# Optimization experiments

Hardware: AMD Instinct MI355X
Metric: run time of the kernel (lower is better)

The kernel has to match this reference:

```python
import jax, jax.numpy as jnp
import numpy as np

N, E, G = 20000, 320000, 64
DIN, H, EF, FC, OUT = 128, 256, 16, 256, 1
BN_EPS = 1e-5


def _gine_layer(x, src, dst, edge_attr, We, be, Wa, ba, g, bt, Wb, bb):
    # GINEConv (eps=0): out = mlp(x + sum_j relu(x_j + lin_edge(e_ij)))
    e = edge_attr @ We.T + be                      # [E, in_ch]
    m = jax.nn.relu(x[src] + e)                    # messages [E, in_ch]
    agg = jax.ops.segment_sum(m, dst, num_segments=x.shape[0])
    h = (x + agg) @ Wa.T + ba                      # Linear
    # BatchNorm1d in eval mode with running_mean=0, running_var=1
    inv = jax.lax.rsqrt(jnp.asarray(1.0 + BN_EPS, h.dtype))
    h = jax.nn.relu(h * inv * g + bt)
    return jax.nn.relu(h @ Wb.T + bb)


def _mean_pool(h, batch, num_graphs):
    sums = jax.ops.segment_sum(h, batch, num_segments=num_graphs)
    cnt = jax.ops.segment_sum(jnp.ones((h.shape[0],), h.dtype), batch, num_segments=num_graphs)
    return sums / jnp.maximum(cnt, 1.0)[:, None]


def setup_inputs() -> dict:
    key = jax.random.key(0)
    ks = iter(jax.random.split(key, 64))

    def nrm(shape, s=0.05):
        return jax.random.normal(next(ks), shape, jnp.float32) * s

    inp = {
        "x": jax.random.normal(next(ks), (N, DIN), jnp.float32),
        "edge_attr": jax.random.normal(next(ks), (E, EF), jnp.float32),
        "src": jax.random.randint(next(ks), (E,), 0, N),
        "dst": jax.random.randint(next(ks), (E,), 0, N),
        "batch": jnp.sort(jax.random.randint(next(ks), (N,), 0, G)),
    }
    dims = [(DIN, H), (H, H), (H, H)]
    for i, (din, h) in enumerate(dims, start=1):
        inp[f"We{i}"] = nrm((din, EF));  inp[f"be{i}"] = jnp.zeros((din,), jnp.float32)
        inp[f"Wa{i}"] = nrm((h, din));  inp[f"ba{i}"] = jnp.zeros((h,), jnp.float32)
        inp[f"g{i}"] = jnp.ones((h,), jnp.float32); inp[f"bt{i}"] = jnp.zeros((h,), jnp.float32)
        inp[f"Wb{i}"] = nrm((h, h));    inp[f"bb{i}"] = jnp.zeros((h,), jnp.float32)
    inp["L1w"] = nrm((FC * 3, H * 3)); inp["L1b"] = jnp.zeros((FC * 3,), jnp.float32)
    inp["L2w"] = nrm((OUT, FC * 3));   inp["L2b"] = jnp.zeros((OUT,), jnp.float32)
    return inp


def reference(x, edge_attr, src, dst, batch,
              We1, be1, Wa1, ba1, g1, bt1, Wb1, bb1,
              We2, be2, Wa2, ba2, g2, bt2, Wb2, bb2,
              We3, be3, Wa3, ba3, g3, bt3, Wb3, bb3,
              L1w, L1b, L2w, L2b):
    h1 = _gine_layer(x,  src, dst, edge_attr, We1, be1, Wa1, ba1, g1, bt1, Wb1, bb1)
    h2 = _gine_layer(h1, src, dst, edge_attr, We2, be2, Wa2, ba2, g2, bt2, Wb2, bb2)
    h3 = _gine_layer(h2, src, dst, edge_attr, We3, be3, Wa3, ba3, g3, bt3, Wb3, bb3)
    p = jnp.concatenate([_mean_pool(h1, batch, G),
                         _mean_pool(h2, batch, G),
                         _mean_pool(h3, batch, G)], axis=1)   # [G, 3H]
    h = jax.nn.relu(p @ L1w.T + L1b)   # dropout is identity (training=False)
    return jax.nn.sigmoid(h @ L2w.T + L2b)
```

## Files before the change

kernel.cpp:

```cpp
#include <hip/hip_runtime.h>
#include <math.h>
#include <stdint.h>

#define N_NODES 20000
#define M_PAD 20032
#define N_EDGES 320000
#define N_GRAPHS 64
#define DIN 128
#define H 256
#define POOL_W 768

typedef __attribute__((ext_vector_type(8))) short bf16x8;
typedef __attribute__((ext_vector_type(4))) float f32x4;
typedef __attribute__((ext_vector_type(4))) unsigned int u32x4;
typedef __attribute__((ext_vector_type(2))) unsigned int u32x2;
typedef _Float16 h2 __attribute__((ext_vector_type(2)));

__device__ __forceinline__ unsigned short f2bf(float f) {
    unsigned u = __builtin_bit_cast(unsigned, f);
    u += 0x7FFFu + ((u >> 16) & 1u);
    return (unsigned short)(u >> 16);
}
__device__ __forceinline__ float bf2f(unsigned short u) {
    return __builtin_bit_cast(float, (unsigned)u << 16);
}
__device__ __forceinline__ unsigned short f2h(float f) {
    const _Float16 h = (_Float16)f;
    return __builtin_bit_cast(unsigned short, h);
}

#if __has_builtin(__builtin_amdgcn_fdot2)
#define DOT2(a, b, c) __builtin_amdgcn_fdot2((a), (b), (c), false)
#else
__device__ __forceinline__ float dot2_fallback(h2 a, h2 b, float c) {
    return fmaf((float)a.x, (float)b.x, fmaf((float)a.y, (float)b.y, c));
}
#define DOT2(a, b, c) dot2_fallback((a), (b), (c))
#endif

struct CvtJob  { const float* s; unsigned short* d; int n4; int mode; };
struct CvtJobs { CvtJob j[13]; };

__global__ __launch_bounds__(256) void cvt_all(CvtJobs jobs)
{
    const CvtJob J = jobs.j[blockIdx.y];
    if (J.mode == 2) {
        const ushort4 z = {0, 0, 0, 0};
        for (int i = blockIdx.x * 256 + threadIdx.x; i < J.n4; i += gridDim.x * 256)
            ((ushort4*)J.d)[i] = z;
        return;
    }
    if (J.mode == 1) {
        for (int i = blockIdx.x * 256 + threadIdx.x; i < J.n4; i += gridDim.x * 256) {
            const float4 v = ((const float4*)J.s)[i];
            ushort4 r;
            r.x = f2h(v.x); r.y = f2h(v.y); r.z = f2h(v.z); r.w = f2h(v.w);
            ((ushort4*)J.d)[i] = r;
        }
        return;
    }
    for (int i = blockIdx.x * 256 + threadIdx.x; i < J.n4; i += gridDim.x * 256) {
        const float4 v = ((const float4*)J.s)[i];
        ushort4 r;
        r.x = f2bf(v.x); r.y = f2bf(v.y); r.z = f2bf(v.z); r.w = f2bf(v.w);
        ((ushort4*)J.d)[i] = r;
    }
}

__global__ __launch_bounds__(256) void hist_kernel(const int* __restrict__ dst,
                                                   int* __restrict__ deg)
{
    const int i = blockIdx.x * 256 + threadIdx.x;
    if (i < N_EDGES) atomicAdd(deg + dst[i], 1);
}

__global__ __launch_bounds__(1024) void scan_kernel(const int* __restrict__ deg,
                                                    int* __restrict__ off,
                                                    int* __restrict__ cur,
                                                    const int* __restrict__ batch,
                                                    int* __restrict__ start)
{
    __shared__ int wsum[16];
    __shared__ int carry;
    const int tid = threadIdx.x, wave = tid >> 6, lane = tid & 63;
    if (tid == 0) carry = 0;
    __syncthreads();
    for (int base = 0; base < N_NODES; base += 1024) {
        const int i = base + tid;
        const int v = (i < N_NODES) ? deg[i] : 0;
        int s = v;
#pragma unroll
        for (int d = 1; d < 64; d <<= 1) {
            const int t = __shfl_up(s, d);
            if (lane >= d) s += t;
        }
        if (lane == 63) wsum[wave] = s;
        __syncthreads();
        if (wave == 0) {
            int t = (lane < 16) ? wsum[lane] : 0;
#pragma unroll
            for (int d = 1; d < 16; d <<= 1) {
                const int u = __shfl_up(t, d);
                if (lane >= d) t += u;
            }
            if (lane < 16) wsum[lane] = t;
        }
        __syncthreads();
        const int wbase = (wave == 0) ? 0 : wsum[wave - 1];
        if (i < N_NODES) {
            const int o = carry + wbase + s - v;
            off[i] = o;
            cur[i] = o;
        }
        const int tot = wsum[15];
        __syncthreads();
        if (tid == 0) carry += tot;
        __syncthreads();
    }
    if (tid == 0) off[N_NODES] = carry;

    if (tid <= N_GRAPHS) {
        if (tid == N_GRAPHS) { start[N_GRAPHS] = N_NODES; }
        else {
            int lo = 0, hi = N_NODES;
            while (lo < hi) { const int mid = (lo + hi) >> 1; if (batch[mid] < tid) lo = mid + 1; else hi = mid; }
            start[tid] = lo;
        }
    }
}

__global__ __launch_bounds__(256) void scatter_kernel(
    const int* __restrict__ src, const int* __restrict__ dst,
    int* __restrict__ cursor, int2* __restrict__ sidx)
{
    const int e = blockIdx.x * 256 + threadIdx.x;
    if (e < N_EDGES) {
        const int p = atomicAdd(cursor + dst[e], 1);
        sidx[p] = make_int2(src[e], e);
    }
}

template<int IN>
__global__ __launch_bounds__(256, 4) void agg3(
    const unsigned short* __restrict__ xb,
    const unsigned short* __restrict__ eah,
    const int2* __restrict__ sidx,
    const int* __restrict__ off,
    const unsigned short* __restrict__ Weh,
    const float* __restrict__ be,
    unsigned short* __restrict__ out)
{
    constexpr int CPL = IN / 64;
    constexpr int XW  = CPL / 2;
    const int lane = threadIdx.x & 63;
    const int node = blockIdx.x * 4 + (threadIdx.x >> 6);
    if (node >= N_NODES) return;
    const int c0 = lane * CPL;
    const int zd = __builtin_amdgcn_mbcnt_lo(0u, 0u);
    const u32x2* sv = (const u32x2*)sidx;

    u32x4 wlo[CPL], whi[CPL];
    float bias[CPL], acc[CPL];
#pragma unroll
    for (int j = 0; j < CPL; ++j) {
        const u32x4* wr = (const u32x4*)(Weh + (size_t)(c0 + j) * 16);
        wlo[j] = wr[0];
        whi[j] = wr[1];
        bias[j] = be[c0 + j];
        acc[j]  = 0.0f;
    }
#pragma unroll
    for (int j = 0; j < CPL; ++j) {
#pragma unroll
        for (int k = 0; k < 4; ++k) {
            { float t = __builtin_bit_cast(float, wlo[j][k]); asm("" : "+v"(t)); wlo[j][k] = __builtin_bit_cast(unsigned int, t); }
            { float t = __builtin_bit_cast(float, whi[j][k]); asm("" : "+v"(t)); whi[j][k] = __builtin_bit_cast(unsigned int, t); }
        }
        asm("" : "+v"(bias[j]));
    }

    const int p0 = __builtin_amdgcn_readfirstlane(off[node]);
    const int p1 = __builtin_amdgcn_readfirstlane(off[node + 1]);
    const int n  = p1 - p0;

    auto ldx = [&](u32x2 id) -> u32x2 {
        const int s = (int)id[0];
        if constexpr (XW == 2) {
            return *(const u32x2*)(xb + (size_t)s * IN + c0);
        } else {
            u32x2 r;
            r[0] = *(const unsigned int*)(xb + (size_t)s * IN + c0);
            r[1] = 0u;
            return r;
        }
    };
    auto ldeaL = [&](u32x2 id) -> u32x4 {
        return ((const u32x4*)(eah + (size_t)id[1] * 16))[0];
    };
    auto ldeaH = [&](u32x2 id) -> u32x4 {
        return ((const u32x4*)(eah + (size_t)id[1] * 16))[1];
    };
    auto ldid = [&](int i) -> u32x2 {
        const int q = (i < n) ? i : (n - 1);
        return sv[p0 + q + zd];
    };
    auto edge_compute = [&](u32x4 eL, u32x4 eH, u32x2 xw) {
        float m[CPL];
#pragma unroll
        for (int j = 0; j < CPL; ++j) m[j] = bias[j];
#pragma unroll
        for (int k = 0; k < 4; ++k) {
            const h2 ep = __builtin_bit_cast(h2, eL[k]);
#pragma unroll
            for (int j = 0; j < CPL; ++j)
                m[j] = DOT2(ep, __builtin_bit_cast(h2, wlo[j][k]), m[j]);
        }
#pragma unroll
        for (int k = 0; k < 4; ++k) {
            const h2 ep = __builtin_bit_cast(h2, eH[k]);
#pragma unroll
            for (int j = 0; j < CPL; ++j)
                m[j] = DOT2(ep, __builtin_bit_cast(h2, whi[j][k]), m[j]);
        }
#pragma unroll
        for (int j = 0; j < CPL; ++j) {
            const unsigned int word = xw[j >> 1];
            const float xf = __builtin_bit_cast(float,
                (j & 1) ? (word & 0xFFFF0000u) : (word << 16));
            acc[j] += fmaxf(m[j] + xf, 0.0f);
        }
    };

    if (n > 0) {
        u32x2 idA = ldid(0), idB = ldid(1);
        u32x2 idC = ldid(2), idD = ldid(3);
        u32x4 eLA = ldeaL(idA), eHA = ldeaH(idA); u32x2 xA = ldx(idA);
        u32x4 eLB = ldeaL(idB), eHB = ldeaH(idB); u32x2 xB = ldx(idB);

        int i = 0;
        for (; i + 2 <= n; i += 2) {
            edge_compute(eLA, eHA, xA);
            eLA = ldeaL(idC); eHA = ldeaH(idC); xA = ldx(idC);
            idC = ldid(i + 4);
            edge_compute(eLB, eHB, xB);
            eLB = ldeaL(idD); eHB = ldeaH(idD); xB = ldx(idD);
            idD = ldid(i + 5);
        }
        if (i < n) edge_compute(eLA, eHA, xA);
    }

    if constexpr (XW == 2) {
        const u32x2 xs = *(const u32x2*)(xb + (size_t)node * IN + c0);
        const float x0 = __builtin_bit_cast(float, xs[0] << 16);
        const float x1 = __builtin_bit_cast(float, xs[0] & 0xFFFF0000u);
        const float x2 = __builtin_bit_cast(float, xs[1] << 16);
        const float x3 = __builtin_bit_cast(float, xs[1] & 0xFFFF0000u);
        u32x2 o;
        o[0] = (unsigned)f2bf(x0 + acc[0]) | ((unsigned)f2bf(x1 + acc[1]) << 16);
        o[1] = (unsigned)f2bf(x2 + acc[2]) | ((unsigned)f2bf(x3 + acc[3]) << 16);
        *(u32x2*)(out + (size_t)node * IN + c0) = o;
    } else {
        const unsigned int xs = *(const unsigned int*)(xb + (size_t)node * IN + c0);
        const float x0 = __builtin_bit_cast(float, xs << 16);
        const float x1 = __builtin_bit_cast(float, xs & 0xFFFF0000u);
        const unsigned int o =
            (unsigned)f2bf(x0 + acc[0]) | ((unsigned)f2bf(x1 + acc[1]) << 16);
        *(unsigned int*)(out + (size_t)node * IN + c0) = o;
    }
}

template<int K, int EPI>
__global__ __launch_bounds__(256) void gemm_breg2(
    const unsigned short* __restrict__ A,
    const unsigned short* __restrict__ W,
    const float* __restrict__ bias,
    const float* __restrict__ gsc, const float* __restrict__ bsh,
    unsigned short* __restrict__ out)
{
    constexpr int KC = K / 32;
    const int w = threadIdx.x >> 6, lane = threadIdx.x & 63;
    const int lm = lane & 15, lq = lane >> 4;
    const int n0 = (blockIdx.y * 4 + w) * 32;
    const int m0 = blockIdx.x * 64;

    bf16x8 B0[KC], B1[KC];
    {
        const unsigned short* Wp0 = W + (size_t)(n0 + lm) * K + lq * 8;
        const unsigned short* Wp1 = W + (size_t)(n0 + 16 + lm) * K + lq * 8;
#pragma unroll
        for (int c = 0; c < KC; ++c) {
            B0[c] = *(const bf16x8*)(Wp0 + c * 32);
            B1[c] = *(const bf16x8*)(Wp1 + c * 32);
        }
    }

    const float inv = rsqrtf(1.0f + 1e-5f);
    const float bc0 = bias[n0 + lm],      bc1 = bias[n0 + 16 + lm];
    const float gc0 = (EPI == 0) ? gsc[n0 + lm]      : 0.0f;
    const float gc1 = (EPI == 0) ? gsc[n0 + 16 + lm] : 0.0f;
    const float sc0 = (EPI == 0) ? bsh[n0 + lm]      : 0.0f;
    const float sc1 = (EPI == 0) ? bsh[n0 + 16 + lm] : 0.0f;

    bf16x8 aC[KC], aN[KC];
    {
        const unsigned short* Ap = A + (size_t)(m0 + lm) * K + lq * 8;
#pragma unroll
        for (int c = 0; c < KC; ++c) aC[c] = *(const bf16x8*)(Ap + c * 32);
    }

#pragma unroll
    for (int ch = 0; ch < 4; ++ch) {
        if (ch < 3) {
            const unsigned short* Ap = A + (size_t)(m0 + (ch + 1) * 16 + lm) * K + lq * 8;
#pragma unroll
            for (int c = 0; c < KC; ++c) aN[c] = *(const bf16x8*)(Ap + c * 32);
        }

        f32x4 acc0 = (f32x4){0.f, 0.f, 0.f, 0.f};
        f32x4 acc1 = (f32x4){0.f, 0.f, 0.f, 0.f};
#pragma unroll
        for (int c = 0; c < KC; ++c) {
            acc0 = __builtin_amdgcn_mfma_f32_16x16x32_bf16(aC[c], B0[c], acc0, 0, 0, 0);
            acc1 = __builtin_amdgcn_mfma_f32_16x16x32_bf16(aC[c], B1[c], acc1, 0, 0, 0);
        }

        const int mr = m0 + ch * 16;
#pragma unroll
        for (int r = 0; r < 4; ++r) {
            const int row = mr + lq * 4 + r;
            if (EPI == 1 && row >= N_NODES) continue;
            float v0 = acc0[r] + bc0;
            float v1 = acc1[r] + bc1;
            if (EPI == 0) {
                v0 = fmaxf(v0 * inv * gc0 + sc0, 0.0f);
                v1 = fmaxf(v1 * inv * gc1 + sc1, 0.0f);
            } else {
                v0 = fmaxf(v0, 0.0f);
                v1 = fmaxf(v1, 0.0f);
            }
            out[(size_t)row * H + n0 + lm]      = f2bf(v0);
            out[(size_t)row * H + n0 + 16 + lm] = f2bf(v1);
        }

#pragma unroll
        for (int c = 0; c < KC; ++c) aC[c] = aN[c];
    }
}

#define RSPLIT 6
__global__ __launch_bounds__(256) void pool2(
    const unsigned short* __restrict__ h1, const unsigned short* __restrict__ h2,
    const unsigned short* __restrict__ h3, const int* __restrict__ start,
    float* __restrict__ pool)
{
    const int g = blockIdx.x & 63, layer = blockIdx.x >> 6;
    const unsigned short* h = (layer == 0) ? h1 : (layer == 1) ? h2 : h3;
    const int r0 = start[g], r1 = start[g + 1];
    const int nr = r1 - r0;
    if (nr <= 0) return;
    const int chunk = (nr + RSPLIT - 1) / RSPLIT;
    const int rs = r0 + blockIdx.y * chunk;
    const int re = (rs + chunk < r1) ? rs + chunk : r1;
    if (rs >= re) return;

    const int c = threadIdx.x;
    float s0 = 0.f, s1 = 0.f, s2 = 0.f, s3 = 0.f;
    int r = rs;
    for (; r + 4 <= re; r += 4) {
        s0 += bf2f(h[(size_t)(r + 0) * H + c]);
        s1 += bf2f(h[(size_t)(r + 1) * H + c]);
        s2 += bf2f(h[(size_t)(r + 2) * H + c]);
        s3 += bf2f(h[(size_t)(r + 3) * H + c]);
    }
    for (; r < re; ++r) s0 += bf2f(h[(size_t)r * H + c]);
    atomicAdd(&pool[(size_t)g * POOL_W + layer * 256 + c], s0 + s1 + s2 + s3);
}

__global__ __launch_bounds__(256) void fc_head(
    const float* __restrict__ pool, const int* __restrict__ start,
    const float* __restrict__ L1w, const float* __restrict__ L1b,
    const float* __restrict__ L2w, float* __restrict__ gsum)
{
    const int g = blockIdx.x;
    __shared__ float p[POOL_W];

    const float rc = 1.0f / fmaxf((float)(start[g + 1] - start[g]), 1.0f);
    for (int i = threadIdx.x; i < POOL_W; i += 256)
        p[i] = pool[(size_t)g * POOL_W + i] * rc;
    __syncthreads();

    const int wv = threadIdx.x >> 6, lane = threadIdx.x & 63;
    const float4* p4 = (const float4*)p;
    const float4 pa = p4[lane], pb = p4[lane + 64], pc = p4[lane + 128];

    const int ob = blockIdx.y * 64 + wv * 16;
    float part = 0.0f;
#pragma unroll 4
    for (int t = 0; t < 16; ++t) {
        const int o = ob + t;
        const float4* wr = (const float4*)(L1w + (size_t)o * POOL_W);
        const float4 a = wr[lane], b = wr[lane + 64], c = wr[lane + 128];
        float acc = a.x * pa.x + a.y * pa.y + a.z * pa.z + a.w * pa.w
                  + b.x * pb.x + b.y * pb.y + b.z * pb.z + b.w * pb.w
                  + c.x * pc.x + c.y * pc.y + c.z * pc.z + c.w * pc.w;
#pragma unroll
        for (int off = 32; off > 0; off >>= 1) acc += __shfl_xor(acc, off);
        if (lane == 0) part += fmaxf(acc + L1b[o], 0.0f) * L2w[o];
    }
    if (lane == 0) atomicAdd(&gsum[g], part);
}

__global__ __launch_bounds__(64) void sig_kernel(
    const float* __restrict__ gsum, const float* __restrict__ L2b,
    float* __restrict__ out)
{
    const int g = threadIdx.x;
    if (g < N_GRAPHS) out[g] = 1.0f / (1.0f + expf(-(gsum[g] + L2b[0])));
}

extern "C" void kernel_launch(void* const* d_in, const int* in_sizes, int n_in,
                              void* d_out, int out_size, void* d_ws, size_t ws_size,
                              hipStream_t stream)
{
    const float* x     = (const float*)d_in[0];
    const float* ea    = (const float*)d_in[1];
    const int*   src   = (const int*)d_in[2];
    const int*   dst   = (const int*)d_in[3];
    const int*   batch = (const int*)d_in[4];

    const float* We[3]; const float* be[3]; const float* Wa[3]; const float* ba[3];
    const float* gg[3]; const float* bt[3]; const float* Wb[3]; const float* bb[3];
    for (int l = 0; l < 3; ++l) {
        const int o = 5 + 8 * l;
        We[l] = (const float*)d_in[o + 0]; be[l] = (const float*)d_in[o + 1];
        Wa[l] = (const float*)d_in[o + 2]; ba[l] = (const float*)d_in[o + 3];
        gg[l] = (const float*)d_in[o + 4]; bt[l] = (const float*)d_in[o + 5];
        Wb[l] = (const float*)d_in[o + 6]; bb[l] = (const float*)d_in[o + 7];
    }
    const float* L1w = (const float*)d_in[29];
    const float* L1b = (const float*)d_in[30];
    const float* L2w = (const float*)d_in[31];
    const float* L2b = (const float*)d_in[32];

    float* pool   = (float*)d_ws;
    float* gsum   = pool + (size_t)N_GRAPHS * POOL_W;
    int*   deg    = (int*)(gsum + N_GRAPHS);
    int*   off    = deg + N_NODES;
    int*   cursor = off + N_NODES + 1;
    int*   start  = cursor + N_NODES;
    int2*  sidx   = (int2*)((((uintptr_t)(start + 72)) + 15) & ~(uintptr_t)15);
    unsigned short* xb = (unsigned short*)((((uintptr_t)(sidx + N_EDGES)) + 15) & ~(uintptr_t)15);
    unsigned short* u  = xb + (size_t)M_PAD * DIN;
    unsigned short* tT = u  + (size_t)M_PAD * H;
    unsigned short* h1 = tT + (size_t)M_PAD * H;
    unsigned short* h2 = h1 + (size_t)M_PAD * H;
    unsigned short* h3 = h2 + (size_t)M_PAD * H;
    unsigned short* wbf[6];
    wbf[0] = h3 + (size_t)M_PAD * H;
    wbf[1] = wbf[0] + H * DIN;
    for (int i = 2; i < 6; ++i) wbf[i] = wbf[i - 1] + H * H;
    unsigned short* eah = wbf[5] + H * H;
    unsigned short* weh[3];
    weh[0] = eah + (size_t)N_EDGES * 16;
    weh[1] = weh[0] + DIN * 16;
    weh[2] = weh[1] + H * 16;

    CvtJobs jobs;
    jobs.j[0]  = { x,       xb,                    N_NODES * DIN / 4,       0 };
    jobs.j[1]  = { Wa[0],   wbf[0],                H * DIN / 4,             0 };
    jobs.j[2]  = { Wb[0],   wbf[1],                H * H / 4,               0 };
    jobs.j[3]  = { Wa[1],   wbf[2],                H * H / 4,               0 };
    jobs.j[4]  = { Wb[1],   wbf[3],                H * H / 4,               0 };
    jobs.j[5]  = { Wa[2],   wbf[4],                H * H / 4,               0 };
    jobs.j[6]  = { Wb[2],   wbf[5],                H * H / 4,               0 };
    jobs.j[7]  = { nullptr, (unsigned short*)deg,  N_NODES * 4 / 8,         2 };
    jobs.j[8]  = { nullptr, (unsigned short*)pool, (N_GRAPHS * POOL_W + N_GRAPHS) * 4 / 8, 2 };
    jobs.j[9]  = { ea,      eah,                   N_EDGES * 16 / 4,        1 };
    jobs.j[10] = { We[0],   weh[0],                DIN * 16 / 4,            1 };
    jobs.j[11] = { We[1],   weh[1],                H * 16 / 4,              1 };
    jobs.j[12] = { We[2],   weh[2],                H * 16 / 4,              1 };
    cvt_all<<<dim3(320, 13), 256, 0, stream>>>(jobs);

    hist_kernel<<<(N_EDGES + 255) / 256, 256, 0, stream>>>(dst, deg);
    scan_kernel<<<1, 1024, 0, stream>>>(deg, off, cursor, batch, start);
    scatter_kernel<<<(N_EDGES + 255) / 256, 256, 0, stream>>>(src, dst, cursor, sidx);

    const int  agrid = (N_NODES + 3) / 4;
    const dim3 ggrid(M_PAD / 64, 2);

    agg3<DIN><<<agrid, 256, 0, stream>>>(xb, eah, sidx, off, weh[0], be[0], u);
    gemm_breg2<DIN, 0><<<ggrid, 256, 0, stream>>>(u, wbf[0], ba[0], gg[0], bt[0], tT);
    gemm_breg2<H,   1><<<ggrid, 256, 0, stream>>>(tT, wbf[1], bb[0], nullptr, nullptr, h1);
    agg3<H><<<agrid, 256, 0, stream>>>(h1, eah, sidx, off, weh[1], be[1], u);
    gemm_breg2<H, 0><<<ggrid, 256, 0, stream>>>(u, wbf[2], ba[1], gg[1], bt[1], tT);
    gemm_breg2<H, 1><<<ggrid, 256, 0, stream>>>(tT, wbf[3], bb[1], nullptr, nullptr, h2);
    agg3<H><<<agrid, 256, 0, stream>>>(h2, eah, sidx, off, weh[2], be[2], u);
    gemm_breg2<H, 0><<<ggrid, 256, 0, stream>>>(u, wbf[4], ba[2], gg[2], bt[2], tT);
    gemm_breg2<H, 1><<<ggrid, 256, 0, stream>>>(tT, wbf[5], bb[2], nullptr, nullptr, h3);

    pool2<<<dim3(3 * N_GRAPHS, RSPLIT), 256, 0, stream>>>(h1, h2, h3, start, pool);
    fc_head<<<dim3(N_GRAPHS, POOL_W / 64), 256, 0, stream>>>(pool, start, L1w, L1b, L2w, gsum);
    sig_kernel<<<1, 64, 0, stream>>>(gsum, L2b, (float*)d_out);
}
```

Before: 530.1 us.

## Store edge features in dst-sorted order during scatter and deepen aggregation prefetch

The scatter kernel now writes the src index and fp16-converted edge attributes directly into destination-sorted order, replacing the separate (src, edge id) index array and the standalone edge-attribute conversion job. Aggregation then reads edge features contiguously instead of gathering them by edge id, and the software pipeline grows from two to four edges in flight. This removes a random gather per edge in each of three layers but makes the scatter write scattered 32-byte rows. It also raises register pressure in the aggregation kernel.

```diff
diff --git a/kernel.cpp b/kernel.cpp
--- a/kernel.cpp
+++ b/kernel.cpp
@@ -39,7 +39,7 @@
 #endif
 
 struct CvtJob  { const float* s; unsigned short* d; int n4; int mode; };
-struct CvtJobs { CvtJob j[13]; };
+struct CvtJobs { CvtJob j[12]; };
 
 __global__ __launch_bounds__(256) void cvt_all(CvtJobs jobs)
 {
@@ -131,20 +131,31 @@
 
 __global__ __launch_bounds__(256) void scatter_kernel(
     const int* __restrict__ src, const int* __restrict__ dst,
-    int* __restrict__ cursor, int2* __restrict__ sidx)
+    const float* __restrict__ ea, int* __restrict__ cursor,
+    int* __restrict__ ssrc, unsigned short* __restrict__ eas)
 {
     const int e = blockIdx.x * 256 + threadIdx.x;
     if (e < N_EDGES) {
         const int p = atomicAdd(cursor + dst[e], 1);
-        sidx[p] = make_int2(src[e], e);
+        ssrc[p] = src[e];
+        const float4* er = (const float4*)(ea + (size_t)e * 16);
+        unsigned short* dr = eas + (size_t)p * 16;
+        ushort4* d4 = (ushort4*)dr;
+#pragma unroll
+        for (int q = 0; q < 4; ++q) {
+            const float4 v = er[q];
+            ushort4 r;
+            r.x = f2h(v.x); r.y = f2h(v.y); r.z = f2h(v.z); r.w = f2h(v.w);
+            d4[q] = r;
+        }
     }
 }
 
 template<int IN>
 __global__ __launch_bounds__(256, 4) void agg3(
     const unsigned short* __restrict__ xb,
-    const unsigned short* __restrict__ eah,
-    const int2* __restrict__ sidx,
+    const unsigned short* __restrict__ eas,
+    const int* __restrict__ ssrc,
     const int* __restrict__ off,
     const unsigned short* __restrict__ Weh,
     const float* __restrict__ be,
@@ -157,7 +168,6 @@
     if (node >= N_NODES) return;
     const int c0 = lane * CPL;
     const int zd = __builtin_amdgcn_mbcnt_lo(0u, 0u);
-    const u32x2* sv = (const u32x2*)sidx;
 
     u32x4 wlo[CPL], whi[CPL];
     float bias[CPL], acc[CPL];
@@ -173,18 +183,29 @@
     for (int j = 0; j < CPL; ++j) {
 #pragma unroll
         for (int k = 0; k < 4; ++k) {
-            { float t = __builtin_bit_cast(float, wlo[j][k]); asm("" : "+v"(t)); wlo[j][k] = __builtin_bit_cast(unsigned int, t); }
-            { float t = __builtin_bit_cast(float, whi[j][k]); asm("" : "+v"(t)); whi[j][k] = __builtin_bit_cast(unsigned int, t); }
-        }
-        asm("" : "+v"(bias[j]));
+            { float t = __builtin_bit_cast(float, wlo[j][k]); asm volatile("" : "+v"(t)); wlo[j][k] = __builtin_bit_cast(unsigned int, t); }
+            { float t = __builtin_bit_cast(float, whi[j][k]); asm volatile("" : "+v"(t)); whi[j][k] = __builtin_bit_cast(unsigned int, t); }
+        }
+        asm volatile("" : "+v"(bias[j]));
     }
 
     const int p0 = __builtin_amdgcn_readfirstlane(off[node]);
     const int p1 = __builtin_amdgcn_readfirstlane(off[node + 1]);
     const int n  = p1 - p0;
 
-    auto ldx = [&](u32x2 id) -> u32x2 {
-        const int s = (int)id[0];
+    auto ldsrc = [&](int i) -> int {
+        const int q = (i < n) ? i : (n - 1);
+        return ssrc[p0 + q + zd];
+    };
+    auto ldeL = [&](int i) -> u32x4 {
+        const int q = (i < n) ? i : (n - 1);
+        return ((const u32x4*)(eas + (size_t)(p0 + q + zd) * 16))[0];
+    };
+    auto ldeH = [&](int i) -> u32x4 {
+        const int q = (i < n) ? i : (n - 1);
+        return ((const u32x4*)(eas + (size_t)(p0 + q + zd) * 16))[1];
+    };
+    auto ldx = [&](int s) -> u32x2 {
         if constexpr (XW == 2) {
             return *(const u32x2*)(xb + (size_t)s * IN + c0);
         } else {
@@ -194,16 +215,6 @@
             return r;
         }
     };
-    auto ldeaL = [&](u32x2 id) -> u32x4 {
-        return ((const u32x4*)(eah + (size_t)id[1] * 16))[0];
-    };
-    auto ldeaH = [&](u32x2 id) -> u32x4 {
-        return ((const u32x4*)(eah + (size_t)id[1] * 16))[1];
-    };
-    auto ldid = [&](int i) -> u32x2 {
-        const int q = (i < n) ? i : (n - 1);
-        return sv[p0 + q + zd];
-    };
     auto edge_compute = [&](u32x4 eL, u32x4 eH, u32x2 xw) {
         float m[CPL];
 #pragma unroll
@@ -232,21 +243,28 @@
     };
 
     if (n > 0) {
-        u32x2 idA = ldid(0), idB = ldid(1);
-        u32x2 idC = ldid(2), idD = ldid(3);
-        u32x4 eLA = ldeaL(idA), eHA = ldeaH(idA); u32x2 xA = ldx(idA);
-        u32x4 eLB = ldeaL(idB), eHB = ldeaH(idB); u32x2 xB = ldx(idB);
+        int sA = ldsrc(0), sB = ldsrc(1), sC = ldsrc(2), sD = ldsrc(3);
+        u32x4 eLA = ldeL(0), eHA = ldeH(0);
+        u32x4 eLB = ldeL(1), eHB = ldeH(1);
+        u32x4 eLC = ldeL(2), eHC = ldeH(2);
+        u32x4 eLD = ldeL(3), eHD = ldeH(3);
+        u32x2 xA = ldx(sA), xB = ldx(sB), xC = ldx(sC), xD = ldx(sD);
+        sA = ldsrc(4); sB = ldsrc(5); sC = ldsrc(6); sD = ldsrc(7);
 
         int i = 0;
-        for (; i + 2 <= n; i += 2) {
+        for (; i + 4 <= n; i += 4) {
             edge_compute(eLA, eHA, xA);
-            eLA = ldeaL(idC); eHA = ldeaH(idC); xA = ldx(idC);
-            idC = ldid(i + 4);
+            eLA = ldeL(i + 4); eHA = ldeH(i + 4); xA = ldx(sA); sA = ldsrc(i + 8);
             edge_compute(eLB, eHB, xB);
-            eLB = ldeaL(idD); eHB = ldeaH(idD); xB = ldx(idD);
-            idD = ldid(i + 5);
-        }
-        if (i < n) edge_compute(eLA, eHA, xA);
+            eLB = ldeL(i + 5); eHB = ldeH(i + 5); xB = ldx(sB); sB = ldsrc(i + 9);
+            edge_compute(eLC, eHC, xC);
+            eLC = ldeL(i + 6); eHC = ldeH(i + 6); xC = ldx(sC); sC = ldsrc(i + 10);
+            edge_compute(eLD, eHD, xD);
+            eLD = ldeL(i + 7); eHD = ldeH(i + 7); xD = ldx(sD); sD = ldsrc(i + 11);
+        }
+        if (i < n)     edge_compute(eLA, eHA, xA);
+        if (i + 1 < n) edge_compute(eLB, eHB, xB);
+        if (i + 2 < n) edge_compute(eLC, eHC, xC);
     }
 
     if constexpr (XW == 2) {
@@ -448,8 +466,9 @@
     int*   off    = deg + N_NODES;
     int*   cursor = off + N_NODES + 1;
     int*   start  = cursor + N_NODES;
-    int2*  sidx   = (int2*)((((uintptr_t)(start + 72)) + 15) & ~(uintptr_t)15);
-    unsigned short* xb = (unsigned short*)((((uintptr_t)(sidx + N_EDGES)) + 15) & ~(uintptr_t)15);
+    int*   ssrc   = (int*)((((uintptr_t)(start + 72)) + 31) & ~(uintptr_t)31);
+    unsigned short* eas = (unsigned short*)((((uintptr_t)(ssrc + N_EDGES)) + 31) & ~(uintptr_t)31);
+    unsigned short* xb = (unsigned short*)((((uintptr_t)(eas + (size_t)N_EDGES * 16)) + 31) & ~(uintptr_t)31);
     unsigned short* u  = xb + (size_t)M_PAD * DIN;
     unsigned short* tT = u  + (size_t)M_PAD * H;
     unsigned short* h1 = tT + (size_t)M_PAD * H;
@@ -459,9 +478,8 @@
     wbf[0] = h3 + (size_t)M_PAD * H;
     wbf[1] = wbf[0] + H * DIN;
     for (int i = 2; i < 6; ++i) wbf[i] = wbf[i - 1] + H * H;
-    unsigned short* eah = wbf[5] + H * H;
     unsigned short* weh[3];
-    weh[0] = eah + (size_t)N_EDGES * 16;
+    weh[0] = wbf[5] + H * H;
     weh[1] = weh[0] + DIN * 16;
     weh[2] = weh[1] + H * 16;
 
@@ -475,26 +493,25 @@
     jobs.j[6]  = { Wb[2],   wbf[5],                H * H / 4,               0 };
     jobs.j[7]  = { nullptr, (unsigned short*)deg,  N_NODES * 4 / 8,         2 };
     jobs.j[8]  = { nullptr, (unsigned short*)pool, (N_GRAPHS * POOL_W + N_GRAPHS) * 4 / 8, 2 };
-    jobs.j[9]  = { ea,      eah,                   N_EDGES * 16 / 4,        1 };
-    jobs.j[10] = { We[0],   weh[0],                DIN * 16 / 4,            1 };
-    jobs.j[11] = { We[1],   weh[1],                H * 16 / 4,              1 };
-    jobs.j[12] = { We[2],   weh[2],                H * 16 / 4,              1 };
-    cvt_all<<<dim3(320, 13), 256, 0, stream>>>(jobs);
+    jobs.j[9]  = { We[0],   weh[0],                DIN * 16 / 4,            1 };
+    jobs.j[10] = { We[1],   weh[1],                H * 16 / 4,              1 };
+    jobs.j[11] = { We[2],   weh[2],                H * 16 / 4,              1 };
+    cvt_all<<<dim3(320, 12), 256, 0, stream>>>(jobs);
 
     hist_kernel<<<(N_EDGES + 255) / 256, 256, 0, stream>>>(dst, deg);
     scan_kernel<<<1, 1024, 0, stream>>>(deg, off, cursor, batch, start);
-    scatter_kernel<<<(N_EDGES + 255) / 256, 256, 0, stream>>>(src, dst, cursor, sidx);
+    scatter_kernel<<<(N_EDGES + 255) / 256, 256, 0, stream>>>(src, dst, ea, cursor, ssrc, eas);
 
     const int  agrid = (N_NODES + 3) / 4;
     const dim3 ggrid(M_PAD / 64, 2);
 
-    agg3<DIN><<<agrid, 256, 0, stream>>>(xb, eah, sidx, off, weh[0], be[0], u);
+    agg3<DIN><<<agrid, 256, 0, stream>>>(xb, eas, ssrc, off, weh[0], be[0], u);
     gemm_breg2<DIN, 0><<<ggrid, 256, 0, stream>>>(u, wbf[0], ba[0], gg[0], bt[0], tT);
     gemm_breg2<H,   1><<<ggrid, 256, 0, stream>>>(tT, wbf[1], bb[0], nullptr, nullptr, h1);
-    agg3<H><<<agrid, 256, 0, stream>>>(h1, eah, sidx, off, weh[1], be[1], u);
+    agg3<H><<<agrid, 256, 0, stream>>>(h1, eas, ssrc, off, weh[1], be[1], u);
     gemm_breg2<H, 0><<<ggrid, 256, 0, stream>>>(u, wbf[2], ba[1], gg[1], bt[1], tT);
     gemm_breg2<H, 1><<<ggrid, 256, 0, stream>>>(tT, wbf[3], bb[1], nullptr, nullptr, h2);
-    agg3<H><<<agrid, 256, 0, stream>>>(h2, eah, sidx, off, weh[2], be[2], u);
+    agg3<H><<<agrid, 256, 0, stream>>>(h2, eas, ssrc, off, weh[2], be[2], u);
     gemm_breg2<H, 0><<<ggrid, 256, 0, stream>>>(u, wbf[4], ba[2], gg[2], bt[2], tT);
     gemm_breg2<H, 1><<<ggrid, 256, 0, stream>>>(tT, wbf[5], bb[2], nullptr, nullptr, h3);
 
```

Measured after the change: 518.3 us. 2.2% less time.
